# Kernel optimization log

Measured on AMD Instinct MI355X. Metric: run time of the kernel, lower is better.

Reference implementation:

```python
import jax, jax.numpy as jnp
import numpy as np

B, S, D = 2, 2048, 2048
H, KVH = 16, 4
HD = D // H  # 128


def _rope_angles(seq, head_dim):
    theta = 1.0 / (10000.0 ** (jnp.arange(0, head_dim, 2, dtype=jnp.float32) / head_dim))
    ang = jnp.arange(seq, dtype=jnp.float32)[:, None] * theta[None, :]  # [S, HD/2]
    return jnp.cos(ang), jnp.sin(ang)


def _apply_rotary(t, cos, sin):
    # t: [B, S, h, HD]; pairs are (even, odd) along last dim (view_as_complex semantics)
    tr = t[..., 0::2]
    ti = t[..., 1::2]
    c = cos[None, :, None, :]
    s = sin[None, :, None, :]
    out_r = tr * c - ti * s
    out_i = tr * s + ti * c
    return jnp.stack([out_r, out_i], axis=-1).reshape(t.shape)


def setup_inputs() -> dict:
    key = jax.random.key(0)
    ks = jax.random.split(key, 8)
    sd = 1.0 / np.sqrt(D)
    return {
        'x': jax.random.normal(ks[0], (B, S, D), dtype=jnp.float32),
        'wq': jax.random.normal(ks[1], (D, D), dtype=jnp.float32) * sd,
        'bq': jax.random.normal(ks[2], (D,), dtype=jnp.float32) * 0.01,
        'wk': jax.random.normal(ks[3], (D, KVH * HD), dtype=jnp.float32) * sd,
        'bk': jax.random.normal(ks[4], (KVH * HD,), dtype=jnp.float32) * 0.01,
        'wv': jax.random.normal(ks[5], (D, KVH * HD), dtype=jnp.float32) * sd,
        'bv': jax.random.normal(ks[6], (KVH * HD,), dtype=jnp.float32) * 0.01,
        'wo': jax.random.normal(ks[7], (D, D), dtype=jnp.float32) * sd,
    }


def reference(x, wq, bq, wk, bk, wv, bv, wo):
    b, s, d = x.shape
    q = (x @ wq + bq).reshape(b, s, H, HD)
    k = (x @ wk + bk).reshape(b, s, KVH, HD)
    v = (x @ wv + bv).reshape(b, s, KVH, HD)

    cos, sin = _rope_angles(s, HD)
    q = _apply_rotary(q, cos, sin)
    k = _apply_rotary(k, cos, sin)

    repeat = H // KVH
    k = jnp.repeat(k, repeat, axis=2)  # [B, S, H, HD]
    v = jnp.repeat(v, repeat, axis=2)

    scale = 1.0 / np.sqrt(HD)
    att_score = jnp.einsum('bqhd,bkhd->bqhk', q, k) * scale  # [B, S, H, S]
    att_weight = jax.nn.softmax(att_score, axis=-1)
    out = jnp.einsum('bqhk,bkhd->bqhd', att_weight, v)
    out = out.reshape(b, s, H * HD)
    return out @ wo
```

## Files before the change

### kernel.cpp

```cpp
#include <hip/hip_runtime.h>
#include <hip/hip_bf16.h>
#include <cstdint>

typedef __attribute__((ext_vector_type(4))) float f32x4;
typedef __attribute__((ext_vector_type(16))) float f32x16;
typedef __attribute__((ext_vector_type(8))) short bf16x8;
typedef __attribute__((ext_vector_type(4))) unsigned int u32x4;
typedef unsigned short u16;
typedef unsigned int u32;

__device__ __forceinline__ u16 f2b(float x) {
  __hip_bfloat16 h = __float2bfloat16(x);
  return *reinterpret_cast<u16*>(&h);
}

__device__ __forceinline__ float b2f(u32 u) {
  u32 v = u << 16;
  return __builtin_bit_cast(float, v);
}

__device__ __forceinline__ u32 pk(float a, float b) {
  __hip_bfloat162 h2 = __float22bfloat162_rn(float2{a, b});
  return *reinterpret_cast<u32*>(&h2);
}

__device__ __forceinline__ void gload16(const void* g, void* l) {
  __builtin_amdgcn_global_load_lds((const __attribute__((address_space(1))) u32*)g,
                                   (__attribute__((address_space(3))) u32*)l, 16, 0, 0);
}

__device__ __forceinline__ float xmax32(float x) {
  return fmaxf(x, __shfl_xor(x, 32, 64));
}
__device__ __forceinline__ float xsum32(float x) {
  return x + __shfl_xor(x, 32, 64);
}


__global__ void cvt_f32_bf16(const float* __restrict__ in, u16* __restrict__ out, int n4) {
  int idx = (blockIdx.x * 256 + threadIdx.x);
  if (idx < n4) {
    const float4 v = *(const float4*)(in + (size_t)idx * 4);
    u16* o = out + (size_t)idx * 4;
    o[0] = f2b(v.x); o[1] = f2b(v.y); o[2] = f2b(v.z); o[3] = f2b(v.w);
  }
}

__global__ void w_transpose_all(const float* __restrict__ wq, const float* __restrict__ wk,
                                const float* __restrict__ wv, const float* __restrict__ wo,
                                u16* __restrict__ wqkv_t, u16* __restrict__ wo_t) {
  __shared__ float tile[32][33];
  int k0 = blockIdx.x * 32;
  int by = blockIdx.y;
  const float* src; int srcN; int c0; u16* out; int n0;
  if (by < 96) {
    n0 = by * 32; out = wqkv_t;
    if (n0 < 2048)      { src = wq; srcN = 2048; c0 = n0; }
    else if (n0 < 2560) { src = wk; srcN = 512;  c0 = n0 - 2048; }
    else                { src = wv; srcN = 512;  c0 = n0 - 2560; }
  } else {
    n0 = (by - 96) * 32; out = wo_t; src = wo; srcN = 2048; c0 = n0;
  }
  int tx = threadIdx.x & 31, ty = threadIdx.x >> 5;
#pragma unroll
  for (int j = 0; j < 32; j += 8)
    tile[ty + j][tx] = src[(size_t)(k0 + ty + j) * srcN + c0 + tx];
  __syncthreads();
#pragma unroll
  for (int j = 0; j < 32; j += 8)
    out[(size_t)(n0 + ty + j) * 2048 + k0 + tx] = f2b(tile[tx][ty + j]);
}

__global__ void v_transpose_cvt(const u16* __restrict__ qkv, u16* __restrict__ vt) {
  __shared__ u16 tile[32][34];
  int s0 = blockIdx.x * 32;
  int d0 = blockIdx.y * 32;
  int z = blockIdx.z;
  int b = z >> 2, kvh = z & 3;
  int tx = threadIdx.x & 31, ty = threadIdx.x >> 5;
#pragma unroll
  for (int j = 0; j < 32; j += 8)
    tile[ty + j][tx] = qkv[((size_t)(b * 2048 + s0 + ty + j)) * 3072 + 2560 + kvh * 128 + d0 + tx];
  __syncthreads();
#pragma unroll
  for (int j = 0; j < 32; j += 8)
    vt[((size_t)z * 128 + d0 + ty + j) * 2048 + s0 + tx] = tile[tx][ty + j];
}

__global__ void rope_cvt(const u16* __restrict__ qkv, u16* __restrict__ out,
                         int lognh, int col0, float scale) {
  int idx = blockIdx.x * 256 + threadIdx.x;
  int i = idx & 63;
  int nh = 1 << lognh;
  int h = (idx >> 6) & (nh - 1);
  int bs = idx >> (6 + lognh);
  int s = bs & 2047;
  int b = bs >> 11;
  u32 pr = *(const u32*)(qkv + (size_t)bs * 3072 + col0 + h * 128 + 2 * i);
  float tr = b2f(pr & 0xffffu), ti = b2f(pr >> 16);
  float theta = expf(-(float)i * 0.14391156831212787f);
  float ang = (float)s * theta;
  float sv, cv;
  sincosf(ang, &sv, &cv);
  float orr = (tr * cv - ti * sv) * scale;
  float oii = (tr * sv + ti * cv) * scale;
  *(u32*)(out + (((size_t)(b * nh + h) * 2048 + s) * 128 + 2 * i)) = pk(orr, oii);
}

__global__ __launch_bounds__(512, 2) void gemm256_bt(
    const u16* __restrict__ A, const u16* __restrict__ Bt,
    const float* __restrict__ bq, const float* __restrict__ bk,
    const float* __restrict__ bv, u16* __restrict__ C,
    int M, int N, int K, int gx) {
  __shared__ u16 lds[65536];
  const int tid = threadIdx.x, lane = tid & 63;
  const int w = tid >> 6, wr = w >> 2, wc = w & 3;
  const int nb = gridDim.x;
  const int swz = (blockIdx.x & 7) * (nb >> 3) + (blockIdx.x >> 3);
  const int m0 = (swz / gx) * 256, n0 = (swz % gx) * 256;
  const int l15 = lane & 15;
  const int gx16 = ((lane >> 4) * 16) ^ (((l15 >> 1) & 3) << 4);

#define GL(X, kh, bufi, t)                                                      \
  { _Pragma("unroll")                                                           \
    for (int rd = 0; rd < 2; ++rd) {                                            \
      int c = tid + rd * 512;                                                   \
      int row = c >> 2;                                                         \
      int sx = ((c & 3) * 16) ^ (((row >> 1) & 3) << 4);                        \
      const u16* srcp = ((X) ? Bt + (size_t)(n0 + row) * K                      \
                             : A + (size_t)(m0 + row) * K) + (t) * 64 + (kh) * 32; \
      gload16((const char*)srcp + sx,                                           \
              (char*)lds + (bufi) * 65536 + (X) * 32768 + (kh) * 16384 + c * 16); \
    } }

  f32x4 acc[8][4] = {};
  const int NT = K >> 6;

  GL(0, 0, 0, 0) GL(1, 0, 0, 0) GL(0, 1, 0, 0) GL(1, 1, 0, 0)

  for (int t = 0; t < NT; ++t) {
    const int buf = t & 1, nbuf = buf ^ 1;
    const int tn = (t + 1 < NT) ? t + 1 : NT - 1;
    const char* Ab = (const char*)lds + buf * 65536;
    const char* Bb = Ab + 32768;
    bf16x8 af[4], bfr[4];

    asm volatile("s_waitcnt vmcnt(4)" ::: "memory");
    __builtin_amdgcn_s_barrier();
    GL(0, 0, nbuf, tn)
#pragma unroll
    for (int n = 0; n < 4; ++n)
      bfr[n] = *(const bf16x8*)(Bb + (wc * 64 + n * 16 + l15) * 64 + gx16);
#pragma unroll
    for (int m = 0; m < 4; ++m)
      af[m] = *(const bf16x8*)(Ab + (wr * 128 + m * 16 + l15) * 64 + gx16);
    __builtin_amdgcn_s_setprio(1);
#pragma unroll
    for (int m = 0; m < 4; ++m)
#pragma unroll
      for (int n = 0; n < 4; ++n)
        acc[m][n] = __builtin_amdgcn_mfma_f32_16x16x32_bf16(af[m], bfr[n], acc[m][n], 0, 0, 0);
    __builtin_amdgcn_s_setprio(0);

    GL(1, 0, nbuf, tn)
#pragma unroll
    for (int m = 0; m < 4; ++m)
      af[m] = *(const bf16x8*)(Ab + (wr * 128 + (m + 4) * 16 + l15) * 64 + gx16);
    __builtin_amdgcn_s_setprio(1);
#pragma unroll
    for (int m = 0; m < 4; ++m)
#pragma unroll
      for (int n = 0; n < 4; ++n)
        acc[m + 4][n] = __builtin_amdgcn_mfma_f32_16x16x32_bf16(af[m], bfr[n], acc[m + 4][n], 0, 0, 0);
    __builtin_amdgcn_s_setprio(0);

    asm volatile("s_waitcnt vmcnt(4)" ::: "memory");
    __builtin_amdgcn_s_barrier();
    GL(0, 1, nbuf, tn)
#pragma unroll
    for (int n = 0; n < 4; ++n)
      bfr[n] = *(const bf16x8*)(Bb + 16384 + (wc * 64 + n * 16 + l15) * 64 + gx16);
#pragma unroll
    for (int m = 0; m < 4; ++m)
      af[m] = *(const bf16x8*)(Ab + 16384 + (wr * 128 + m * 16 + l15) * 64 + gx16);
    __builtin_amdgcn_s_setprio(1);
#pragma unroll
    for (int m = 0; m < 4; ++m)
#pragma unroll
      for (int n = 0; n < 4; ++n)
        acc[m][n] = __builtin_amdgcn_mfma_f32_16x16x32_bf16(af[m], bfr[n], acc[m][n], 0, 0, 0);
    __builtin_amdgcn_s_setprio(0);

    GL(1, 1, nbuf, tn)
#pragma unroll
    for (int m = 0; m < 4; ++m)
      af[m] = *(const bf16x8*)(Ab + 16384 + (wr * 128 + (m + 4) * 16 + l15) * 64 + gx16);
    __builtin_amdgcn_s_setprio(1);
#pragma unroll
    for (int m = 0; m < 4; ++m)
#pragma unroll
      for (int n = 0; n < 4; ++n)
        acc[m + 4][n] = __builtin_amdgcn_mfma_f32_16x16x32_bf16(af[m], bfr[n], acc[m + 4][n], 0, 0, 0);
    __builtin_amdgcn_s_setprio(0);
  }
  asm volatile("s_waitcnt vmcnt(0)" ::: "memory");

#pragma unroll
  for (int m = 0; m < 8; ++m) {
    int row = m0 + wr * 128 + m * 16 + ((lane >> 4) << 2);
#pragma unroll
    for (int n = 0; n < 4; ++n) {
      int col = n0 + wc * 64 + n * 16 + l15;
      float bvv = (col < 2048) ? bq[col] : ((col < 2560) ? bk[col - 2048] : bv[col - 2560]);
      u16* cp = C + (size_t)row * N + col;
#pragma unroll
      for (int r = 0; r < 4; ++r) cp[(size_t)r * N] = f2b(acc[m][n][r] + bvv);
    }
  }
}

__global__ __launch_bounds__(512, 1) void gemm128x256_bt(
    const u16* __restrict__ A, const u16* __restrict__ Bt,
    float* __restrict__ C, int M, int N, int K, int gx) {
  __shared__ u16 lds[49152];
  const int tid = threadIdx.x, lane = tid & 63;
  const int w = tid >> 6, wr = w >> 2, wc = w & 3;
  const int nb = gridDim.x;
  const int swz = (blockIdx.x & 7) * (nb >> 3) + (blockIdx.x >> 3);
  const int m0 = (swz / gx) * 128, n0 = (swz % gx) * 256;
  const int l15 = lane & 15;
  const int gx16 = ((lane >> 4) * 16) ^ (((l15 >> 1) & 3) << 4);

#define GLA(kh, bufi, t)                                                        \
  { int c = tid;                                                                \
    int row = c >> 2;                                                           \
    int sx = ((c & 3) * 16) ^ (((row >> 1) & 3) << 4);                          \
    const u16* srcp = A + (size_t)(m0 + row) * K + (t) * 64 + (kh) * 32;        \
    gload16((const char*)srcp + sx,                                             \
            (char*)lds + (bufi) * 16384 + (kh) * 8192 + c * 16); }

#define GLB(kh, bufi, t)                                                        \
  { _Pragma("unroll")                                                           \
    for (int rd = 0; rd < 2; ++rd) {                                            \
      int c = tid + rd * 512;                                                   \
      int row = c >> 2;                                                         \
      int sx = ((c & 3) * 16) ^ (((row >> 1) & 3) << 4);                        \
      const u16* srcp = Bt + (size_t)(n0 + row) * K + (t) * 64 + (kh) * 32;     \
      gload16((const char*)srcp + sx,                                           \
              (char*)lds + 32768 + (bufi) * 32768 + (kh) * 16384 + c * 16); } }

  f32x4 acc[4][4] = {};
  const int NT = K >> 6;

  GLA(0, 0, 0) GLB(0, 0, 0) GLA(1, 0, 0) GLB(1, 0, 0)

  for (int t = 0; t < NT; ++t) {
    const int buf = t & 1, nbuf = buf ^ 1;
    const int tn = (t + 1 < NT) ? t + 1 : NT - 1;
    const char* Ab = (const char*)lds + buf * 16384;
    const char* Bb = (const char*)lds + 32768 + buf * 32768;
    bf16x8 af[4], bfr[4];

#pragma unroll
    for (int kh = 0; kh < 2; ++kh) {
      asm volatile("s_waitcnt vmcnt(3)" ::: "memory");
      __builtin_amdgcn_s_barrier();
      if (kh == 0) { GLA(0, nbuf, tn) GLB(0, nbuf, tn) }
      else         { GLA(1, nbuf, tn) GLB(1, nbuf, tn) }
#pragma unroll
      for (int n = 0; n < 4; ++n)
        bfr[n] = *(const bf16x8*)(Bb + kh * 16384 + (wc * 64 + n * 16 + l15) * 64 + gx16);
#pragma unroll
      for (int m = 0; m < 4; ++m)
        af[m] = *(const bf16x8*)(Ab + kh * 8192 + (wr * 64 + m * 16 + l15) * 64 + gx16);
      __builtin_amdgcn_s_setprio(1);
#pragma unroll
      for (int m = 0; m < 4; ++m)
#pragma unroll
        for (int n = 0; n < 4; ++n)
          acc[m][n] = __builtin_amdgcn_mfma_f32_16x16x32_bf16(af[m], bfr[n], acc[m][n], 0, 0, 0);
      __builtin_amdgcn_s_setprio(0);
    }
  }
  asm volatile("s_waitcnt vmcnt(0)" ::: "memory");

#pragma unroll
  for (int m = 0; m < 4; ++m) {
    int row = m0 + wr * 64 + m * 16 + ((lane >> 4) << 2);
#pragma unroll
    for (int n = 0; n < 4; ++n) {
      int col = n0 + wc * 64 + n * 16 + l15;
      float* cp = C + (size_t)row * N + col;
#pragma unroll
      for (int r = 0; r < 4; ++r) cp[(size_t)r * N] = acc[m][n][r];
    }
  }
}

__global__ __launch_bounds__(128, 3) void flash_attn(
    const u16* __restrict__ Qr, const u16* __restrict__ Kr,
    const u16* __restrict__ Vt, u16* __restrict__ Att) {
  __shared__ u16 Ks[2][32 * 128];
  __shared__ u16 Vs[2][128 * 32];
  const int tid = threadIdx.x, lane = tid & 63, w = tid >> 6;
  const int lo = lane & 31, hi = lane >> 5;
  const int q0 = blockIdx.x * 64 + w * 32;
  const int h = blockIdx.y, b = blockIdx.z;
  const int kvh = h >> 2;

  const char* Khead = (const char*)(Kr + (size_t)(b * 4 + kvh) * 2048 * 128);
  const char* Vhead = (const char*)(Vt + (size_t)(b * 4 + kvh) * 128 * 2048);

  bf16x8 qf[8];
  {
    const u16* qp = Qr + ((size_t)(b * 16 + h) * 2048 + q0 + lo) * 128 + hi * 8;
#pragma unroll
    for (int ds = 0; ds < 8; ++ds) qf[ds] = *(const bf16x8*)(qp + ds * 16);
  }

#define STAGE(bufi, t)                                                        \
  {                                                                           \
    _Pragma("unroll")                                                         \
    for (int it = 0; it < 4; ++it) {                                          \
      int c = it * 128 + tid;                                                 \
      int krow = c >> 4;                                                      \
      int koff = krow * 256 + ((c & 15) << 4 ^ ((krow & 7) << 4));            \
      gload16(Khead + (size_t)(t) * 8192 + koff,                              \
              (u16*)Ks[bufi] + it * 1024 + w * 512);                          \
      int vrow = c >> 2;                                                      \
      int voff = vrow * 4096 + ((c & 3) << 4 ^ (((vrow >> 1) & 3) << 4));     \
      gload16(Vhead + (size_t)(t) * 64 + voff,                                \
              (u16*)Vs[bufi] + it * 1024 + w * 512);                          \
    }                                                                         \
  }

  f32x16 o0 = {}, o1 = {}, o2 = {}, o3 = {};
  float m_run = -3.0e38f, l_run = 0.f;
  const int swz = (lo & 7) << 4;
  const int vswz = ((lo >> 1) & 3) << 4;
  const int hi16 = hi * 16;

  STAGE(0, 0);
  __syncthreads();

  int buf = 0;
  for (int t = 0; t < 64; ++t) {
    int tn = (t < 63) ? t + 1 : 63;
    STAGE(buf ^ 1, tn);

    const char* Kb = (const char*)Ks[buf];
    const char* Vb = (const char*)Vs[buf];

    f32x16 sc = {};
    __builtin_amdgcn_s_setprio(1);
#pragma unroll
    for (int ds = 0; ds < 8; ++ds) {
      bf16x8 kf = *(const bf16x8*)(Kb + lo * 256 + ((ds * 32 + hi16) ^ swz));
      sc = __builtin_amdgcn_mfma_f32_32x32x16_bf16(kf, qf[ds], sc, 0, 0, 0);
    }
    __builtin_amdgcn_s_setprio(0);

    float m01 = fmaxf(fmaxf(sc[0], sc[1]), fmaxf(sc[2], sc[3]));
    float m23 = fmaxf(fmaxf(sc[4], sc[5]), fmaxf(sc[6], sc[7]));
    float m45 = fmaxf(fmaxf(sc[8], sc[9]), fmaxf(sc[10], sc[11]));
    float m67 = fmaxf(fmaxf(sc[12], sc[13]), fmaxf(sc[14], sc[15]));
    float pmax = xmax32(fmaxf(fmaxf(m01, m23), fmaxf(m45, m67)));

    if (!__all(pmax - m_run <= 8.0f)) {
      float mnew = fmaxf(m_run, pmax);
      float rs = __expf(m_run - mnew);
      m_run = mnew;
      l_run *= rs;
#pragma unroll
      for (int r = 0; r < 16; ++r) {
        float rsr = __shfl(rs, (r & 3) + 8 * (r >> 2) + 4 * hi, 64);
        o0[r] *= rsr; o1[r] *= rsr; o2[r] *= rsr; o3[r] *= rsr;
      }
    }

    float lsum = 0.f;
#pragma unroll
    for (int r = 0; r < 16; ++r) { float p = __expf(sc[r] - m_run); sc[r] = p; lsum += p; }
    l_run += xsum32(lsum);

    bf16x8 pa0, pa1;
    {
      u32 a0 = pk(sc[0], sc[1]),   a1 = pk(sc[2], sc[3]);
      u32 b0 = pk(sc[4], sc[5]),   b1 = pk(sc[6], sc[7]);
      u32 t0 = hi ? a0 : b0, t1 = hi ? a1 : b1;
      u32 r0 = __shfl_xor(t0, 32, 64), r1 = __shfl_xor(t1, 32, 64);
      u32x4 w0;
      w0[0] = hi ? r0 : a0; w0[1] = hi ? r1 : a1;
      w0[2] = hi ? b0 : r0; w0[3] = hi ? b1 : r1;
      pa0 = __builtin_bit_cast(bf16x8, w0);
      u32 c0 = pk(sc[8], sc[9]),   c1 = pk(sc[10], sc[11]);
      u32 d0 = pk(sc[12], sc[13]), d1 = pk(sc[14], sc[15]);
      u32 t2 = hi ? c0 : d0, t3 = hi ? c1 : d1;
      u32 r2 = __shfl_xor(t2, 32, 64), r3 = __shfl_xor(t3, 32, 64);
      u32x4 w1;
      w1[0] = hi ? r2 : c0; w1[1] = hi ? r3 : c1;
      w1[2] = hi ? d0 : r2; w1[3] = hi ? d1 : r3;
      pa1 = __builtin_bit_cast(bf16x8, w1);
    }

    __builtin_amdgcn_s_setprio(1);
#define PVN(on, n)                                                                                     \
    {                                                                                                  \
      const char* vrb = Vb + ((n) * 32 + lo) * 64;                                                     \
      on = __builtin_amdgcn_mfma_f32_32x32x16_bf16(pa0, *(const bf16x8*)(vrb + ((0  + hi16) ^ vswz)), on, 0, 0, 0); \
      on = __builtin_amdgcn_mfma_f32_32x32x16_bf16(pa1, *(const bf16x8*)(vrb + ((32 + hi16) ^ vswz)), on, 0, 0, 0); \
    }
    PVN(o0, 0)
    PVN(o1, 1)
    PVN(o2, 2)
    PVN(o3, 3)
    __builtin_amdgcn_s_setprio(0);

    __syncthreads();
    buf ^= 1;
  }

  float inv = 1.0f / l_run;
  size_t rowbase = (size_t)(b * 2048 + q0);
#pragma unroll
  for (int r = 0; r < 16; ++r) {
    int rr = (r & 3) + 8 * (r >> 2) + 4 * hi;
    float invr = __shfl(inv, rr, 64);
    u16* op = Att + (rowbase + rr) * 2048 + h * 128 + lo;
    op[0]  = f2b(o0[r] * invr);
    op[32] = f2b(o1[r] * invr);
    op[64] = f2b(o2[r] * invr);
    op[96] = f2b(o3[r] * invr);
  }
}


extern "C" void kernel_launch(void* const* d_in, const int* in_sizes, int n_in,
                              void* d_out, int out_size, void* d_ws, size_t ws_size,
                              hipStream_t stream) {
  const float* x  = (const float*)d_in[0];
  const float* wq = (const float*)d_in[1];
  const float* bq = (const float*)d_in[2];
  const float* wk = (const float*)d_in[3];
  const float* bk = (const float*)d_in[4];
  const float* wv = (const float*)d_in[5];
  const float* bv = (const float*)d_in[6];
  const float* wo = (const float*)d_in[7];
  float* out = (float*)d_out;
  char* ws = (char*)d_ws;

  u16*   x_bf   = (u16*)  (ws + 0);
  u16*   att    = (u16*)  (ws + 0);
  u16*   wqkv_t = (u16*)  (ws + 16777216);
  u16*   wo_t   = (u16*)  (ws + 29360128);
  u16*   qkv    = (u16*)  (ws + 37761024);
  u16*   q_r    = (u16*)  (ws + 88092672);
  u16*   k_r    = (u16*)  (ws + 104869888);
  u16*   v_t    = (u16*)  (ws + 109064192);

  cvt_f32_bf16<<<8192, 256, 0, stream>>>(x, x_bf, 2097152);
  w_transpose_all<<<dim3(64, 160), 256, 0, stream>>>(wq, wk, wv, wo, wqkv_t, wo_t);

  gemm256_bt<<<192, 512, 0, stream>>>(x_bf, wqkv_t, bq, bk, bv, qkv, 4096, 3072, 2048, 12);

  rope_cvt<<<16384, 256, 0, stream>>>(qkv, q_r, 4, 0, 0.08838834764831845f);
  rope_cvt<<<4096, 256, 0, stream>>>(qkv, k_r, 2, 2048, 1.0f);
  v_transpose_cvt<<<dim3(64, 4, 8), 256, 0, stream>>>(qkv, v_t);

  flash_attn<<<dim3(32, 16, 2), 128, 0, stream>>>(q_r, k_r, v_t, att);

  gemm128x256_bt<<<256, 512, 0, stream>>>(att, wo_t, out, 4096, 2048, 2048, 8);
}
```

Baseline: 256.6 us.

## Fuse RoPE, scaling and V transpose into QKV GEMM epilogue

The QKV GEMM epilogue now applies bias, rotary embedding (pairing lanes with a shuffle) and the Q softmax scale, and writes V directly in transposed layout. This removes the three rope_cvt and v_transpose launches and their extra global-memory round trips. Flash attention reads Q and K straight from the strided qkv buffer instead of packed per-head copies. The cost is sincos work inside the GEMM epilogue, more register pressure there, strided 6144-byte-row K loads in attention, and narrow scattered stores for V^T.

Result: slower. 279.6 us (+8.9%).

```diff
diff --git a/kernel.cpp b/kernel.cpp
--- a/kernel.cpp
+++ b/kernel.cpp
@@ -12,11 +12,6 @@
 __device__ __forceinline__ u16 f2b(float x) {
   __hip_bfloat16 h = __float2bfloat16(x);
   return *reinterpret_cast<u16*>(&h);
-}
-
-__device__ __forceinline__ float b2f(u32 u) {
-  u32 v = u << 16;
-  return __builtin_bit_cast(float, v);
 }
 
 __device__ __forceinline__ u32 pk(float a, float b) {
@@ -71,47 +66,11 @@
     out[(size_t)(n0 + ty + j) * 2048 + k0 + tx] = f2b(tile[tx][ty + j]);
 }
 
-__global__ void v_transpose_cvt(const u16* __restrict__ qkv, u16* __restrict__ vt) {
-  __shared__ u16 tile[32][34];
-  int s0 = blockIdx.x * 32;
-  int d0 = blockIdx.y * 32;
-  int z = blockIdx.z;
-  int b = z >> 2, kvh = z & 3;
-  int tx = threadIdx.x & 31, ty = threadIdx.x >> 5;
-#pragma unroll
-  for (int j = 0; j < 32; j += 8)
-    tile[ty + j][tx] = qkv[((size_t)(b * 2048 + s0 + ty + j)) * 3072 + 2560 + kvh * 128 + d0 + tx];
-  __syncthreads();
-#pragma unroll
-  for (int j = 0; j < 32; j += 8)
-    vt[((size_t)z * 128 + d0 + ty + j) * 2048 + s0 + tx] = tile[tx][ty + j];
-}
-
-__global__ void rope_cvt(const u16* __restrict__ qkv, u16* __restrict__ out,
-                         int lognh, int col0, float scale) {
-  int idx = blockIdx.x * 256 + threadIdx.x;
-  int i = idx & 63;
-  int nh = 1 << lognh;
-  int h = (idx >> 6) & (nh - 1);
-  int bs = idx >> (6 + lognh);
-  int s = bs & 2047;
-  int b = bs >> 11;
-  u32 pr = *(const u32*)(qkv + (size_t)bs * 3072 + col0 + h * 128 + 2 * i);
-  float tr = b2f(pr & 0xffffu), ti = b2f(pr >> 16);
-  float theta = expf(-(float)i * 0.14391156831212787f);
-  float ang = (float)s * theta;
-  float sv, cv;
-  sincosf(ang, &sv, &cv);
-  float orr = (tr * cv - ti * sv) * scale;
-  float oii = (tr * sv + ti * cv) * scale;
-  *(u32*)(out + (((size_t)(b * nh + h) * 2048 + s) * 128 + 2 * i)) = pk(orr, oii);
-}
-
 __global__ __launch_bounds__(512, 2) void gemm256_bt(
     const u16* __restrict__ A, const u16* __restrict__ Bt,
     const float* __restrict__ bq, const float* __restrict__ bk,
     const float* __restrict__ bv, u16* __restrict__ C,
-    int M, int N, int K, int gx) {
+    u16* __restrict__ vt, int M, int N, int K, int gx) {
   __shared__ u16 lds[65536];
   const int tid = threadIdx.x, lane = tid & 63;
   const int w = tid >> 6, wr = w >> 2, wc = w & 3;
@@ -205,16 +164,54 @@
   }
   asm volatile("s_waitcnt vmcnt(0)" ::: "memory");
 
-#pragma unroll
-  for (int m = 0; m < 8; ++m) {
-    int row = m0 + wr * 128 + m * 16 + ((lane >> 4) << 2);
+  const int colbase = n0 + wc * 64;
+  if (n0 < 2560) {
+    const float qscale = (n0 < 2048) ? 0.08838834764831845f : 1.0f;
+    const bool evenp = !(l15 & 1);
+    float theta[4];
 #pragma unroll
     for (int n = 0; n < 4; ++n) {
-      int col = n0 + wc * 64 + n * 16 + l15;
-      float bvv = (col < 2048) ? bq[col] : ((col < 2560) ? bk[col - 2048] : bv[col - 2560]);
-      u16* cp = C + (size_t)row * N + col;
-#pragma unroll
-      for (int r = 0; r < 4; ++r) cp[(size_t)r * N] = f2b(acc[m][n][r] + bvv);
+      int col = colbase + n * 16 + l15;
+      theta[n] = expf(-(float)((col & 127) >> 1) * 0.14391156831212787f);
+    }
+#pragma unroll
+    for (int m = 0; m < 8; ++m) {
+      int row = m0 + wr * 128 + m * 16 + ((lane >> 4) << 2);
+#pragma unroll
+      for (int n = 0; n < 4; ++n) {
+        int col = colbase + n * 16 + l15;
+        float bvv = (col < 2048) ? bq[col] : bk[col - 2048];
+        u16* cp = C + (size_t)row * N + col;
+#pragma unroll
+        for (int r = 0; r < 4; ++r) {
+          float v = acc[m][n][r] + bvv;
+          float o = __shfl_xor(v, 1, 64);
+          float ang = (float)((row + r) & 2047) * theta[n];
+          float sn, cs;
+          sincosf(ang, &sn, &cs);
+          float res = evenp ? (v * cs - o * sn) : (v * cs + o * sn);
+          cp[(size_t)r * N] = f2b(res * qscale);
+        }
+      }
+    }
+  } else {
+#pragma unroll
+    for (int m = 0; m < 8; ++m) {
+      int row = m0 + wr * 128 + m * 16 + ((lane >> 4) << 2);
+      int b = row >> 11, s = row & 2047;
+#pragma unroll
+      for (int n = 0; n < 4; ++n) {
+        int col = colbase + n * 16 + l15;
+        int c = col - 2560;
+        float bvv = bv[c];
+        u16* vp = vt + ((size_t)(b * 4 + (c >> 7)) * 128 + (c & 127)) * 2048 + s;
+        ushort4 st;
+        st.x = f2b(acc[m][n][0] + bvv);
+        st.y = f2b(acc[m][n][1] + bvv);
+        st.z = f2b(acc[m][n][2] + bvv);
+        st.w = f2b(acc[m][n][3] + bvv);
+        *(ushort4*)vp = st;
+      }
     }
   }
 }
@@ -298,8 +295,7 @@
 }
 
 __global__ __launch_bounds__(128, 3) void flash_attn(
-    const u16* __restrict__ Qr, const u16* __restrict__ Kr,
-    const u16* __restrict__ Vt, u16* __restrict__ Att) {
+    const u16* __restrict__ qkv, const u16* __restrict__ Vt, u16* __restrict__ Att) {
   __shared__ u16 Ks[2][32 * 128];
   __shared__ u16 Vs[2][128 * 32];
   const int tid = threadIdx.x, lane = tid & 63, w = tid >> 6;
@@ -308,12 +304,12 @@
   const int h = blockIdx.y, b = blockIdx.z;
   const int kvh = h >> 2;
 
-  const char* Khead = (const char*)(Kr + (size_t)(b * 4 + kvh) * 2048 * 128);
+  const char* Khead = (const char*)qkv + ((size_t)b * 2048 * 3072 + 2048 + kvh * 128) * 2;
   const char* Vhead = (const char*)(Vt + (size_t)(b * 4 + kvh) * 128 * 2048);
 
   bf16x8 qf[8];
   {
-    const u16* qp = Qr + ((size_t)(b * 16 + h) * 2048 + q0 + lo) * 128 + hi * 8;
+    const u16* qp = qkv + (size_t)(b * 2048 + q0 + lo) * 3072 + h * 128 + hi * 8;
 #pragma unroll
     for (int ds = 0; ds < 8; ++ds) qf[ds] = *(const bf16x8*)(qp + ds * 16);
   }
@@ -324,8 +320,8 @@
     for (int it = 0; it < 4; ++it) {                                          \
       int c = it * 128 + tid;                                                 \
       int krow = c >> 4;                                                      \
-      int koff = krow * 256 + ((c & 15) << 4 ^ ((krow & 7) << 4));            \
-      gload16(Khead + (size_t)(t) * 8192 + koff,                              \
+      int koff = ((c & 15) << 4) ^ ((krow & 7) << 4);                         \
+      gload16(Khead + (size_t)((t) * 32 + krow) * 6144 + koff,                \
               (u16*)Ks[bufi] + it * 1024 + w * 512);                          \
       int vrow = c >> 2;                                                      \
       int voff = vrow * 4096 + ((c & 3) << 4 ^ (((vrow >> 1) & 3) << 4));     \
@@ -454,20 +450,15 @@
   u16*   wqkv_t = (u16*)  (ws + 16777216);
   u16*   wo_t   = (u16*)  (ws + 29360128);
   u16*   qkv    = (u16*)  (ws + 37761024);
-  u16*   q_r    = (u16*)  (ws + 88092672);
-  u16*   k_r    = (u16*)  (ws + 104869888);
   u16*   v_t    = (u16*)  (ws + 109064192);
 
   cvt_f32_bf16<<<8192, 256, 0, stream>>>(x, x_bf, 2097152);
   w_transpose_all<<<dim3(64, 160), 256, 0, stream>>>(wq, wk, wv, wo, wqkv_t, wo_t);
 
-  gemm256_bt<<<192, 512, 0, stream>>>(x_bf, wqkv_t, bq, bk, bv, qkv, 4096, 3072, 2048, 12);
-
-  rope_cvt<<<16384, 256, 0, stream>>>(qkv, q_r, 4, 0, 0.08838834764831845f);
-  rope_cvt<<<4096, 256, 0, stream>>>(qkv, k_r, 2, 2048, 1.0f);
-  v_transpose_cvt<<<dim3(64, 4, 8), 256, 0, stream>>>(qkv, v_t);
-
-  flash_attn<<<dim3(32, 16, 2), 128, 0, stream>>>(q_r, k_r, v_t, att);
+  gemm256_bt<<<192, 512, 0, stream>>>(x_bf, wqkv_t, bq, bk, bv, qkv, v_t,
+                                      4096, 3072, 2048, 12);
+
+  flash_attn<<<dim3(32, 16, 2), 128, 0, stream>>>(qkv, v_t, att);
 
   gemm128x256_bt<<<256, 512, 0, stream>>>(att, wo_t, out, 4096, 2048, 2048, 8);
 }
```
